# Kernel tuning notes

Hardware: AMD Instinct MI355X
Metric: run time of the kernel (lower is better)

## Reference

```python
import jax, jax.numpy as jnp
import numpy as np

B, T, D, E = 4, 1024, 1024, 8
HD = 4 * D  # hdim = 4*dim


def setup_inputs() -> dict:
    key = jax.random.key(0)
    k1, k2, k3, k4 = jax.random.split(key, 4)
    std = 0.5 * D ** (-0.5)
    bound = (3.0 ** 0.5) * std
    x = jax.random.normal(k1, (B, T, D), dtype=jnp.float32)
    # router zero-init in source; use small random weights so routing is non-degenerate
    router_w = jax.random.normal(k2, (E, D), dtype=jnp.float32) * 0.02
    expert_fc = jax.random.uniform(k3, (E, D, HD), dtype=jnp.float32, minval=-bound, maxval=bound)
    # proj zero-init in source; use small random so output/backward are non-trivial
    expert_proj = jax.random.normal(k4, (E, D, HD), dtype=jnp.float32) * 0.02
    return {"x": x, "router_w": router_w, "expert_fc": expert_fc, "expert_proj": expert_proj}


def reference(x, router_w, expert_fc, expert_proj):
    # router: Linear(dim, E, bias=False) -> logits [B,T,E]
    logits = jnp.einsum('btd,ed->bte', x, router_w)
    probs = jax.nn.softmax(logits, axis=-1)
    expert_ids = jnp.argmax(probs, axis=-1)  # [B,T]; top-1 (max) routing
    # NOTE: source computes expert_weights (max prob) but does NOT use it in combine.
    mask = jax.nn.one_hot(expert_ids, E, dtype=x.dtype)  # [B,T,E]
    # Dense all-experts compute (faithful to source): h = x @ fc (F.linear with fc.T)
    h = jnp.einsum('btd,edh->ebth', x, expert_fc)
    h = jnp.square(jax.nn.relu(h))  # relu(h)**2
    # expert_output = h @ proj.T (F.linear with proj [dim, hdim])
    out_e = jnp.einsum('ebth,edh->ebtd', h, expert_proj)
    # masked combine: sum_e out_e * (ids == e)
    output = jnp.einsum('ebtd,bte->btd', out_e, mask)
    return output
```

## Files before the change

kernel.cpp:

```cpp
#include <hip/hip_runtime.h>
#include <hip/hip_bf16.h>
#include <stdint.h>

#define NE 8
#define DIM 1024
#define HDIM 4096
#define NTOK 4096
#define KSPLIT 4
#define MAXT 40

typedef unsigned short ushort_t;
typedef __attribute__((ext_vector_type(4))) float f32x4;
typedef __attribute__((ext_vector_type(8))) short bf16x8;

__device__ __forceinline__ ushort_t f2b(float f) {
  union { float f; unsigned u; } c; c.f = f;
  unsigned u = c.u;
  return (ushort_t)((u + 0x7fffu + ((u >> 16) & 1u)) >> 16);
}

__device__ __forceinline__ bf16x8 cvt8(const float* p) {
  f32x4 lo = *(const f32x4*)p;
  f32x4 hi = *(const f32x4*)(p + 4);
  union { unsigned u[4]; bf16x8 v; } r;
  union { float f; unsigned u; } a, b;
  a.f = lo[0]; b.f = lo[1]; r.u[0] = __builtin_amdgcn_perm(b.u, a.u, 0x07060302);
  a.f = lo[2]; b.f = lo[3]; r.u[1] = __builtin_amdgcn_perm(b.u, a.u, 0x07060302);
  a.f = hi[0]; b.f = hi[1]; r.u[2] = __builtin_amdgcn_perm(b.u, a.u, 0x07060302);
  a.f = hi[2]; b.f = hi[3]; r.u[3] = __builtin_amdgcn_perm(b.u, a.u, 0x07060302);
  return r.v;
}

__device__ __forceinline__ void gl2lds16(const void* g, void* l) {
  __builtin_amdgcn_global_load_lds(
      (__attribute__((address_space(1))) void*)g,
      (__attribute__((address_space(3))) void*)l, 16, 0, 0);
}

__global__ __launch_bounds__(256) void router_kernel(
    const float* __restrict__ x, const float* __restrict__ rw,
    int* __restrict__ eid, int* __restrict__ rank, int* __restrict__ cnt) {
  __shared__ float w[NE * 1028];
  for (int i = threadIdx.x; i < NE * DIM; i += 256) {
    int e = i >> 10, d = i & 1023;
    w[e * 1028 + d] = rw[i];
  }
  __syncthreads();
  int grp = threadIdx.x >> 3;
  int e = threadIdx.x & 7;
  int t = blockIdx.x * 32 + grp;
  const float4* xr = (const float4*)(x + (size_t)t * DIM);
  const float4* wr = (const float4*)(w + e * 1028);
  float acc = 0.f;
#pragma unroll 4
  for (int i = 0; i < DIM / 4; ++i) {
    float4 xv = xr[i], wv = wr[i];
    acc += xv.x * wv.x + xv.y * wv.y + xv.z * wv.z + xv.w * wv.w;
  }
  float v = acc; int ie = e;
#pragma unroll
  for (int m = 4; m; m >>= 1) {
    float ov = __shfl_xor(v, m, 8);
    int oi = __shfl_xor(ie, m, 8);
    if (ov > v || (ov == v && oi < ie)) { v = ov; ie = oi; }
  }
  if (e == 0) {
    eid[t] = ie;
    rank[t] = atomicAdd(&cnt[ie], 1);
  }
}

__global__ void scan_kernel(const int* __restrict__ cnt, int* __restrict__ offs,
                            int* __restrict__ tile_e, int* __restrict__ tile_m,
                            int* __restrict__ ntiles) {
  if (threadIdx.x == 0) {
    int s = 0, nt = 0;
    for (int e = 0; e < NE; ++e) {
      offs[e] = s;
      int c = cnt[e];
      for (int m = 0; m < c; m += 128) { tile_e[nt] = e; tile_m[nt] = m; ++nt; }
      s += c;
    }
    offs[NE] = s;
    *ntiles = nt;
  }
}

__global__ __launch_bounds__(256) void gather_kernel(
    const float* __restrict__ x, const int* __restrict__ eid,
    const int* __restrict__ rank, const int* __restrict__ offs,
    int* __restrict__ sorted, ushort_t* __restrict__ Xg) {
  int t = blockIdx.x;
  int e = eid[t];
  int pos = offs[e] + rank[t];
  if (threadIdx.x == 0) sorted[pos] = t;
  int i = threadIdx.x;
  float4 v = ((const float4*)(x + (size_t)t * DIM))[i];
  ushort4 o = make_ushort4(f2b(v.x), f2b(v.y), f2b(v.z), f2b(v.w));
  *(ushort4*)(Xg + (size_t)pos * DIM + i * 4) = o;
}

__global__ __launch_bounds__(256) void transpose_fc_kernel(
    const float* __restrict__ fc, ushort_t* __restrict__ fct) {
  __shared__ float tile[32][33];
  int e = blockIdx.z;
  int h0 = blockIdx.x * 32, d0 = blockIdx.y * 32;
  int c = threadIdx.x & 31, r0 = threadIdx.x >> 5;
  const float* src = fc + ((size_t)e * DIM + d0) * HDIM + h0 + c;
#pragma unroll
  for (int i = 0; i < 4; ++i) {
    int r = r0 + i * 8;
    tile[r][c] = src[(size_t)r * HDIM];
  }
  __syncthreads();
  ushort_t* dst = fct + ((size_t)e * HDIM + h0) * DIM + d0 + c;
#pragma unroll
  for (int i = 0; i < 4; ++i) {
    int r = r0 + i * 8;
    dst[(size_t)r * DIM] = f2b(tile[c][r]);
  }
}

__global__ __launch_bounds__(256, 2) void gemm1_kernel(
    const ushort_t* __restrict__ Xg, const ushort_t* __restrict__ fct,
    const int* __restrict__ offs, const int* __restrict__ tile_e,
    const int* __restrict__ tile_m, const int* __restrict__ ntiles,
    ushort_t* __restrict__ H) {
  if ((int)blockIdx.y >= *ntiles) return;
  int e = tile_e[blockIdx.y];
  int mb = tile_m[blockIdx.y];
  int m0 = offs[e];
  int Me = offs[e + 1] - m0;
  int n0 = blockIdx.x * 128;

  __shared__ ushort_t As[128 * 32];
  __shared__ ushort_t Bs[128 * 32];

  int tid = threadIdx.x;
  int wave = tid >> 6;
  int lane = tid & 63;

  const ushort_t* ap[2]; const ushort_t* bp[2];
  ushort_t* al[2]; ushort_t* bl[2];
#pragma unroll
  for (int q = 0; q < 2; ++q) {
    int rl = (wave * 2 + q) * 16 + (lane >> 2);
    int kc = (lane & 3) * 8;
    int rg = mb + rl; if (rg >= Me) rg = Me - 1;
    ap[q] = Xg + (size_t)(m0 + rg) * DIM + kc;
    bp[q] = fct + ((size_t)e * HDIM + n0 + rl) * DIM + kc;
    al[q] = &As[(wave * 2 + q) * 512];
    bl[q] = &Bs[(wave * 2 + q) * 512];
  }

  f32x4 acc[4][4] = {};
  int wm = (wave & 1) * 64;
  int wn = (wave >> 1) * 64;
  int fr = lane & 15;
  int kq = (lane >> 4) * 8;

  for (int k0 = 0; k0 < DIM; k0 += 32) {
    gl2lds16(ap[0] + k0, al[0]);
    gl2lds16(ap[1] + k0, al[1]);
    gl2lds16(bp[0] + k0, bl[0]);
    gl2lds16(bp[1] + k0, bl[1]);
    __syncthreads();
    bf16x8 af[4], bf[4];
#pragma unroll
    for (int i = 0; i < 4; ++i) {
      af[i] = *(const bf16x8*)&As[(wm + i * 16 + fr) * 32 + kq];
      bf[i] = *(const bf16x8*)&Bs[(wn + i * 16 + fr) * 32 + kq];
    }
#pragma unroll
    for (int i = 0; i < 4; ++i)
#pragma unroll
      for (int j = 0; j < 4; ++j)
        acc[i][j] = __builtin_amdgcn_mfma_f32_16x16x32_bf16(af[i], bf[j], acc[i][j], 0, 0, 0);
    __syncthreads();
  }

  int cq = (lane >> 4) * 4;
#pragma unroll
  for (int i = 0; i < 4; ++i) {
#pragma unroll
    for (int r = 0; r < 4; ++r) {
      int rl = wm + i * 16 + cq + r;
      int rg = mb + rl;
      if (rg < Me) {
        ushort_t* dst = H + (size_t)(m0 + rg) * HDIM + n0 + wn + (lane & 15);
#pragma unroll
        for (int j = 0; j < 4; ++j) {
          float v = acc[i][j][r];
          v = fmaxf(v, 0.f);
          dst[j * 16] = f2b(v * v);
        }
      }
    }
  }
}

__global__ __launch_bounds__(256, 2) void gemm2_kernel(
    const ushort_t* __restrict__ Hm, const float* __restrict__ pj,
    const int* __restrict__ offs, const int* __restrict__ tile_e,
    const int* __restrict__ tile_m, const int* __restrict__ ntiles,
    float* __restrict__ P) {
  if ((int)blockIdx.y >= *ntiles) return;
  int e = tile_e[blockIdx.y];
  int mb = tile_m[blockIdx.y];
  int ks = blockIdx.z;
  int m0 = offs[e];
  int Me = offs[e + 1] - m0;
  int n0 = blockIdx.x * 128;

  __shared__ ushort_t As[128 * 32];
  __shared__ float Bs[128 * 36];

  int tid = threadIdx.x;
  int wave = tid >> 6;
  int lane = tid & 63;

  const ushort_t* ap[2]; ushort_t* al[2];
#pragma unroll
  for (int q = 0; q < 2; ++q) {
    int rl = (wave * 2 + q) * 16 + (lane >> 2);
    int kc = (lane & 3) * 8;
    int rg = mb + rl; if (rg >= Me) rg = Me - 1;
    ap[q] = Hm + (size_t)(m0 + rg) * HDIM + kc;
    al[q] = &As[(wave * 2 + q) * 512];
  }

  const float* bsrc[4]; float* bdst[4];
#pragma unroll
  for (int p = 0; p < 4; ++p) {
    int row = p * 32 + (tid >> 3);
    int ch = tid & 7;
    bsrc[p] = pj + ((size_t)e * DIM + n0 + row) * HDIM + ch * 4;
    bdst[p] = &Bs[row * 36 + ch * 4];
  }

  f32x4 acc[4][4] = {};
  int wm = (wave & 1) * 64;
  int wn = (wave >> 1) * 64;
  int fr = lane & 15;
  int kq = (lane >> 4) * 8;

  int kbeg = ks * (HDIM / KSPLIT);
  int kend = kbeg + (HDIM / KSPLIT);
  for (int k0 = kbeg; k0 < kend; k0 += 32) {
    gl2lds16(ap[0] + k0, al[0]);
    gl2lds16(ap[1] + k0, al[1]);
    float4 bv[4];
#pragma unroll
    for (int p = 0; p < 4; ++p) bv[p] = *(const float4*)(bsrc[p] + k0);
#pragma unroll
    for (int p = 0; p < 4; ++p) *(float4*)bdst[p] = bv[p];
    __syncthreads();
    bf16x8 af[4], bf[4];
#pragma unroll
    for (int i = 0; i < 4; ++i) {
      af[i] = *(const bf16x8*)&As[(wm + i * 16 + fr) * 32 + kq];
      bf[i] = cvt8(&Bs[(wn + i * 16 + fr) * 36 + kq]);
    }
#pragma unroll
    for (int i = 0; i < 4; ++i)
#pragma unroll
      for (int j = 0; j < 4; ++j)
        acc[i][j] = __builtin_amdgcn_mfma_f32_16x16x32_bf16(af[i], bf[j], acc[i][j], 0, 0, 0);
    __syncthreads();
  }

  int cq = (lane >> 4) * 4;
#pragma unroll
  for (int i = 0; i < 4; ++i) {
#pragma unroll
    for (int r = 0; r < 4; ++r) {
      int rl = wm + i * 16 + cq + r;
      int rg = mb + rl;
      if (rg < Me) {
        float* dst = P + ((size_t)ks * NTOK + (m0 + rg)) * DIM + n0 + wn + (lane & 15);
#pragma unroll
        for (int j = 0; j < 4; ++j) dst[j * 16] = acc[i][j][r];
      }
    }
  }
}

__global__ __launch_bounds__(256) void reduce_kernel(
    const float* __restrict__ P, const int* __restrict__ sorted,
    float* __restrict__ out) {
  int pos = blockIdx.x;
  int tok = sorted[pos];
  int i = threadIdx.x;
  size_t base = (size_t)pos * DIM + i * 4;
  const size_t S = (size_t)NTOK * DIM;
  f32x4 s = *(const f32x4*)(P + base) + *(const f32x4*)(P + S + base) +
            *(const f32x4*)(P + 2 * S + base) + *(const f32x4*)(P + 3 * S + base);
  *(f32x4*)(out + (size_t)tok * DIM + i * 4) = s;
}

extern "C" void kernel_launch(void* const* d_in, const int* in_sizes, int n_in,
                              void* d_out, int out_size, void* d_ws, size_t ws_size,
                              hipStream_t stream) {
  const float* x  = (const float*)d_in[0];
  const float* rw = (const float*)d_in[1];
  const float* fc = (const float*)d_in[2];
  const float* pj = (const float*)d_in[3];
  float* out = (float*)d_out;
  char* ws = (char*)d_ws;

  int* eid        = (int*)(ws + 0x0000);
  int* rank       = (int*)(ws + 0x4000);
  int* cnt        = (int*)(ws + 0x8000);
  int* offs       = (int*)(ws + 0x8100);
  int* tile_e     = (int*)(ws + 0x8200);
  int* tile_m     = (int*)(ws + 0x8600);
  int* ntiles     = (int*)(ws + 0x8a00);
  int* sorted     = (int*)(ws + 0x9000);
  ushort_t* Xg    = (ushort_t*)(ws + 0x10000);
  ushort_t* H     = (ushort_t*)(ws + 0x810000);
  ushort_t* W     = (ushort_t*)(ws + 0x2810000);
  float* P        = (float*)W;

  hipMemsetAsync(cnt, 0, 32, stream);
  router_kernel<<<NTOK / 32, 256, 0, stream>>>(x, rw, eid, rank, cnt);
  scan_kernel<<<1, 64, 0, stream>>>(cnt, offs, tile_e, tile_m, ntiles);
  gather_kernel<<<NTOK, 256, 0, stream>>>(x, eid, rank, offs, sorted, Xg);
  transpose_fc_kernel<<<dim3(HDIM / 32, DIM / 32, NE), 256, 0, stream>>>(fc, W);
  gemm1_kernel<<<dim3(HDIM / 128, MAXT), 256, 0, stream>>>(Xg, W, offs, tile_e, tile_m, ntiles, H);
  gemm2_kernel<<<dim3(DIM / 128, MAXT, KSPLIT), 256, 0, stream>>>(H, pj, offs, tile_e, tile_m, ntiles, P);
  reduce_kernel<<<NTOK, 256, 0, stream>>>(P, sorted, out);
}
```

Baseline: 490.9 us.

## Double-buffer GEMM LDS tiles and widen transpose to 64x64 vectorized tiles

```diff
diff --git a/kernel.cpp b/kernel.cpp
--- a/kernel.cpp
+++ b/kernel.cpp
@@ -12,6 +12,7 @@
 typedef unsigned short ushort_t;
 typedef __attribute__((ext_vector_type(4))) float f32x4;
 typedef __attribute__((ext_vector_type(8))) short bf16x8;
+typedef __attribute__((ext_vector_type(8))) ushort_t u16x8;
 
 __device__ __forceinline__ ushort_t f2b(float f) {
   union { float f; unsigned u; } c; c.f = f;
@@ -19,16 +20,9 @@
   return (ushort_t)((u + 0x7fffu + ((u >> 16) & 1u)) >> 16);
 }
 
-__device__ __forceinline__ bf16x8 cvt8(const float* p) {
-  f32x4 lo = *(const f32x4*)p;
-  f32x4 hi = *(const f32x4*)(p + 4);
-  union { unsigned u[4]; bf16x8 v; } r;
-  union { float f; unsigned u; } a, b;
-  a.f = lo[0]; b.f = lo[1]; r.u[0] = __builtin_amdgcn_perm(b.u, a.u, 0x07060302);
-  a.f = lo[2]; b.f = lo[3]; r.u[1] = __builtin_amdgcn_perm(b.u, a.u, 0x07060302);
-  a.f = hi[0]; b.f = hi[1]; r.u[2] = __builtin_amdgcn_perm(b.u, a.u, 0x07060302);
-  a.f = hi[2]; b.f = hi[3]; r.u[3] = __builtin_amdgcn_perm(b.u, a.u, 0x07060302);
-  return r.v;
+__device__ __forceinline__ unsigned pk2(float a, float b) {
+  union { float f; unsigned u; } x, y; x.f = a; y.f = b;
+  return __builtin_amdgcn_perm(y.u, x.u, 0x07060302);
 }
 
 __device__ __forceinline__ void gl2lds16(const void* g, void* l) {
@@ -102,23 +96,27 @@
 
 __global__ __launch_bounds__(256) void transpose_fc_kernel(
     const float* __restrict__ fc, ushort_t* __restrict__ fct) {
-  __shared__ float tile[32][33];
+  __shared__ float tile[64][68];
   int e = blockIdx.z;
-  int h0 = blockIdx.x * 32, d0 = blockIdx.y * 32;
-  int c = threadIdx.x & 31, r0 = threadIdx.x >> 5;
-  const float* src = fc + ((size_t)e * DIM + d0) * HDIM + h0 + c;
+  int h0 = blockIdx.x * 64, d0 = blockIdx.y * 64;
+  int tid = threadIdx.x;
+  int rr = tid >> 4;
+  int cc = (tid & 15) * 4;
+  const float* src = fc + ((size_t)e * DIM + d0 + rr) * HDIM + h0 + cc;
 #pragma unroll
   for (int i = 0; i < 4; ++i) {
-    int r = r0 + i * 8;
-    tile[r][c] = src[(size_t)r * HDIM];
+    float4 v = *(const float4*)(src + (size_t)(i * 16) * HDIM);
+    *(float4*)&tile[rr + i * 16][cc] = v;
   }
   __syncthreads();
-  ushort_t* dst = fct + ((size_t)e * HDIM + h0) * DIM + d0 + c;
-#pragma unroll
-  for (int i = 0; i < 4; ++i) {
-    int r = r0 + i * 8;
-    dst[(size_t)r * DIM] = f2b(tile[c][r]);
-  }
+  int hr = tid >> 2;
+  int dseg = (tid & 3) * 16;
+  union { ushort_t s[16]; u16x8 v[2]; } o;
+#pragma unroll
+  for (int j = 0; j < 16; ++j) o.s[j] = f2b(tile[dseg + j][hr]);
+  ushort_t* dst = fct + ((size_t)e * HDIM + h0 + hr) * DIM + d0 + dseg;
+  *(u16x8*)dst = o.v[0];
+  *(u16x8*)(dst + 8) = o.v[1];
 }
 
 __global__ __launch_bounds__(256, 2) void gemm1_kernel(
@@ -133,15 +131,15 @@
   int Me = offs[e + 1] - m0;
   int n0 = blockIdx.x * 128;
 
-  __shared__ ushort_t As[128 * 32];
-  __shared__ ushort_t Bs[128 * 32];
+  __shared__ ushort_t As[2][128 * 32];
+  __shared__ ushort_t Bs[2][128 * 32];
 
   int tid = threadIdx.x;
   int wave = tid >> 6;
   int lane = tid & 63;
 
   const ushort_t* ap[2]; const ushort_t* bp[2];
-  ushort_t* al[2]; ushort_t* bl[2];
+  int soff[2];
 #pragma unroll
   for (int q = 0; q < 2; ++q) {
     int rl = (wave * 2 + q) * 16 + (lane >> 2);
@@ -149,8 +147,7 @@
     int rg = mb + rl; if (rg >= Me) rg = Me - 1;
     ap[q] = Xg + (size_t)(m0 + rg) * DIM + kc;
     bp[q] = fct + ((size_t)e * HDIM + n0 + rl) * DIM + kc;
-    al[q] = &As[(wave * 2 + q) * 512];
-    bl[q] = &Bs[(wave * 2 + q) * 512];
+    soff[q] = (wave * 2 + q) * 512;
   }
 
   f32x4 acc[4][4] = {};
@@ -159,17 +156,26 @@
   int fr = lane & 15;
   int kq = (lane >> 4) * 8;
 
+  gl2lds16(ap[0], &As[0][soff[0]]);
+  gl2lds16(ap[1], &As[0][soff[1]]);
+  gl2lds16(bp[0], &Bs[0][soff[0]]);
+  gl2lds16(bp[1], &Bs[0][soff[1]]);
+  __syncthreads();
+
+  int cur = 0;
   for (int k0 = 0; k0 < DIM; k0 += 32) {
-    gl2lds16(ap[0] + k0, al[0]);
-    gl2lds16(ap[1] + k0, al[1]);
-    gl2lds16(bp[0] + k0, bl[0]);
-    gl2lds16(bp[1] + k0, bl[1]);
-    __syncthreads();
+    int cn = cur ^ 1;
+    if (k0 + 32 < DIM) {
+      gl2lds16(ap[0] + k0 + 32, &As[cn][soff[0]]);
+      gl2lds16(ap[1] + k0 + 32, &As[cn][soff[1]]);
+      gl2lds16(bp[0] + k0 + 32, &Bs[cn][soff[0]]);
+      gl2lds16(bp[1] + k0 + 32, &Bs[cn][soff[1]]);
+    }
     bf16x8 af[4], bf[4];
 #pragma unroll
     for (int i = 0; i < 4; ++i) {
-      af[i] = *(const bf16x8*)&As[(wm + i * 16 + fr) * 32 + kq];
-      bf[i] = *(const bf16x8*)&Bs[(wn + i * 16 + fr) * 32 + kq];
+      af[i] = *(const bf16x8*)&As[cur][(wm + i * 16 + fr) * 32 + kq];
+      bf[i] = *(const bf16x8*)&Bs[cur][(wn + i * 16 + fr) * 32 + kq];
     }
 #pragma unroll
     for (int i = 0; i < 4; ++i)
@@ -177,6 +183,7 @@
       for (int j = 0; j < 4; ++j)
         acc[i][j] = __builtin_amdgcn_mfma_f32_16x16x32_bf16(af[i], bf[j], acc[i][j], 0, 0, 0);
     __syncthreads();
+    cur = cn;
   }
 
   int cq = (lane >> 4) * 4;
@@ -212,31 +219,29 @@
   int Me = offs[e + 1] - m0;
   int n0 = blockIdx.x * 128;
 
-  __shared__ ushort_t As[128 * 32];
-  __shared__ float Bs[128 * 36];
+  __shared__ ushort_t As[2][128 * 32];
+  __shared__ ushort_t Bs[2][128 * 32];
 
   int tid = threadIdx.x;
   int wave = tid >> 6;
   int lane = tid & 63;
 
-  const ushort_t* ap[2]; ushort_t* al[2];
+  const ushort_t* ap[2]; int soff[2];
 #pragma unroll
   for (int q = 0; q < 2; ++q) {
     int rl = (wave * 2 + q) * 16 + (lane >> 2);
     int kc = (lane & 3) * 8;
     int rg = mb + rl; if (rg >= Me) rg = Me - 1;
     ap[q] = Hm + (size_t)(m0 + rg) * HDIM + kc;
-    al[q] = &As[(wave * 2 + q) * 512];
-  }
-
-  const float* bsrc[4]; float* bdst[4];
-#pragma unroll
-  for (int p = 0; p < 4; ++p) {
-    int row = p * 32 + (tid >> 3);
-    int ch = tid & 7;
-    bsrc[p] = pj + ((size_t)e * DIM + n0 + row) * HDIM + ch * 4;
-    bdst[p] = &Bs[row * 36 + ch * 4];
-  }
+    soff[q] = (wave * 2 + q) * 512;
+  }
+
+  int br = tid >> 2;
+  int bk = (tid & 3) * 8;
+  const float* bsrc0 = pj + ((size_t)e * DIM + n0 + br) * HDIM + bk;
+  const float* bsrc1 = bsrc0 + (size_t)64 * HDIM;
+  int boff0 = br * 32 + bk;
+  int boff1 = (br + 64) * 32 + bk;
 
   f32x4 acc[4][4] = {};
   int wm = (wave & 1) * 64;
@@ -246,27 +251,59 @@
 
   int kbeg = ks * (HDIM / KSPLIT);
   int kend = kbeg + (HDIM / KSPLIT);
+
+  float4 bv[4];
+  bv[0] = *(const float4*)(bsrc0 + kbeg);
+  bv[1] = *(const float4*)(bsrc0 + kbeg + 4);
+  bv[2] = *(const float4*)(bsrc1 + kbeg);
+  bv[3] = *(const float4*)(bsrc1 + kbeg + 4);
+  gl2lds16(ap[0] + kbeg, &As[0][soff[0]]);
+  gl2lds16(ap[1] + kbeg, &As[0][soff[1]]);
+  {
+    union { unsigned u[4]; bf16x8 v; } w;
+    w.u[0] = pk2(bv[0].x, bv[0].y); w.u[1] = pk2(bv[0].z, bv[0].w);
+    w.u[2] = pk2(bv[1].x, bv[1].y); w.u[3] = pk2(bv[1].z, bv[1].w);
+    *(bf16x8*)&Bs[0][boff0] = w.v;
+    w.u[0] = pk2(bv[2].x, bv[2].y); w.u[1] = pk2(bv[2].z, bv[2].w);
+    w.u[2] = pk2(bv[3].x, bv[3].y); w.u[3] = pk2(bv[3].z, bv[3].w);
+    *(bf16x8*)&Bs[0][boff1] = w.v;
+  }
+  __syncthreads();
+
+  int cur = 0;
   for (int k0 = kbeg; k0 < kend; k0 += 32) {
-    gl2lds16(ap[0] + k0, al[0]);
-    gl2lds16(ap[1] + k0, al[1]);
-    float4 bv[4];
-#pragma unroll
-    for (int p = 0; p < 4; ++p) bv[p] = *(const float4*)(bsrc[p] + k0);
-#pragma unroll
-    for (int p = 0; p < 4; ++p) *(float4*)bdst[p] = bv[p];
-    __syncthreads();
+    int cn = cur ^ 1;
+    bool more = (k0 + 32) < kend;
+    if (more) {
+      bv[0] = *(const float4*)(bsrc0 + k0 + 32);
+      bv[1] = *(const float4*)(bsrc0 + k0 + 36);
+      bv[2] = *(const float4*)(bsrc1 + k0 + 32);
+      bv[3] = *(const float4*)(bsrc1 + k0 + 36);
+      gl2lds16(ap[0] + k0 + 32, &As[cn][soff[0]]);
+      gl2lds16(ap[1] + k0 + 32, &As[cn][soff[1]]);
+    }
     bf16x8 af[4], bf[4];
 #pragma unroll
     for (int i = 0; i < 4; ++i) {
-      af[i] = *(const bf16x8*)&As[(wm + i * 16 + fr) * 32 + kq];
-      bf[i] = cvt8(&Bs[(wn + i * 16 + fr) * 36 + kq]);
+      af[i] = *(const bf16x8*)&As[cur][(wm + i * 16 + fr) * 32 + kq];
+      bf[i] = *(const bf16x8*)&Bs[cur][(wn + i * 16 + fr) * 32 + kq];
     }
 #pragma unroll
     for (int i = 0; i < 4; ++i)
 #pragma unroll
       for (int j = 0; j < 4; ++j)
         acc[i][j] = __builtin_amdgcn_mfma_f32_16x16x32_bf16(af[i], bf[j], acc[i][j], 0, 0, 0);
+    if (more) {
+      union { unsigned u[4]; bf16x8 v; } w;
+      w.u[0] = pk2(bv[0].x, bv[0].y); w.u[1] = pk2(bv[0].z, bv[0].w);
+      w.u[2] = pk2(bv[1].x, bv[1].y); w.u[3] = pk2(bv[1].z, bv[1].w);
+      *(bf16x8*)&Bs[cn][boff0] = w.v;
+      w.u[0] = pk2(bv[2].x, bv[2].y); w.u[1] = pk2(bv[2].z, bv[2].w);
+      w.u[2] = pk2(bv[3].x, bv[3].y); w.u[3] = pk2(bv[3].z, bv[3].w);
+      *(bf16x8*)&Bs[cn][boff1] = w.v;
+    }
     __syncthreads();
+    cur = cn;
   }
 
   int cq = (lane >> 4) * 4;
@@ -325,7 +362,7 @@
   router_kernel<<<NTOK / 32, 256, 0, stream>>>(x, rw, eid, rank, cnt);
   scan_kernel<<<1, 64, 0, stream>>>(cnt, offs, tile_e, tile_m, ntiles);
   gather_kernel<<<NTOK, 256, 0, stream>>>(x, eid, rank, offs, sorted, Xg);
-  transpose_fc_kernel<<<dim3(HDIM / 32, DIM / 32, NE), 256, 0, stream>>>(fc, W);
+  transpose_fc_kernel<<<dim3(HDIM / 64, DIM / 64, NE), 256, 0, stream>>>(fc, W);
   gemm1_kernel<<<dim3(HDIM / 128, MAXT), 256, 0, stream>>>(Xg, W, offs, tile_e, tile_m, ntiles, H);
   gemm2_kernel<<<dim3(DIM / 128, MAXT, KSPLIT), 256, 0, stream>>>(H, pj, offs, tile_e, tile_m, ntiles, P);
   reduce_kernel<<<NTOK, 256, 0, stream>>>(P, sorted, out);
```

After: 490.6 us. Within noise of the previous version (-0.1%).
